# Optimization experiments

Hardware: AMD Instinct MI355X
Metric: run time of the kernel (lower is better)

Reference implementation:

```python
import jax, jax.numpy as jnp
import numpy as np

B, M, T, R, N_IN, O, K = 2, 20000, 8, 5, 64, 128, 4  # batch, verts, N_theta, N_rho, in, out, kernels


def setup_inputs() -> dict:
    key = jax.random.key(0)
    k1, k2, k3, k4 = jax.random.split(key, 4)
    signal = jax.random.normal(k1, (B, M, N_IN), dtype=jnp.float32)
    u = jax.random.uniform(k2, (B, M, T, R, 3), dtype=jnp.float32, minval=1e-3, maxval=1.0)
    bary_weights = u / jnp.sum(u, axis=-1, keepdims=True)  # barycentric: sum to 1
    bary_indices = jax.random.randint(k3, (B, M, T, R, 3), 0, M, dtype=jnp.int32)
    # glorot-ish scale for (amt_kernel, N_theta, N_rho, out, in) weight tensor
    kernel = jax.random.normal(k4, (K, T, R, O, N_IN), dtype=jnp.float32) * 0.05
    return {"signal": signal, "bary_weights": bary_weights,
            "bary_indices": bary_indices, "kernel": kernel}


def reference(signal, bary_weights, bary_indices, kernel):
    # signal: (B, m, n); bary_weights/indices: (B, m, T, R, 3); kernel: (K, T, R, o, n)
    Ksum = jnp.sum(kernel, axis=0)                      # sum over kernels k: (T, R, o, n)
    T_ = kernel.shape[1]
    j = jnp.arange(T_)
    rot = (j[None, :] + j[:, None]) % T_                # rot[r, j] = (j + r) % T
    Krot = Ksum[rot]                                    # (T_r, T_j, R, o, n)

    def one(sig, w, idx):
        g = sig[idx]                                    # gather: (m, T, R, 3, n)
        x = jnp.einsum('mtrc,mtrcn->mtrn', w, g)        # barycentric pullback (m, T, R, n)
        conv = jnp.einsum('rjion,mjin->rmo', Krot, x)   # per-rotation conv (T_r, m, o)
        a = jax.nn.relu(conv)
        norms = jnp.linalg.norm(a, axis=-1)             # (T_r, m)
        best = jnp.argmax(norms, axis=0)                # (m,)
        return jnp.take_along_axis(a, best[None, :, None], axis=0)[0]  # angular max pool (m, o)

    return jax.vmap(one)(signal, bary_weights, bary_indices)
```

## Files before the change

### kernel.cpp

```cpp
#include <hip/hip_runtime.h>
#include <hip/hip_bf16.h>


typedef _Float16 f16;
typedef _Float16 f16x8 __attribute__((ext_vector_type(8)));
typedef float f32x4 __attribute__((ext_vector_type(4)));

#define B_   2
#define M_   20000
#define T_   8
#define R_   5
#define NIN  64
#define O_   128
#define K_   4

#define PTS   (B_*M_)
#define PTSPAD 40192
#define KSEG  2560
#define KPHY  5120
#define KLOG  7680
#define NQ    1024
#define SCALE 16.0f
#define INVSS (1.0f/(SCALE*SCALE))

#define BM    256
#define BK    64
#define TS    (KLOG/BK)

__global__ void k_ksum(const float* __restrict__ kern, float* __restrict__ ksum) {
    int i = blockIdx.x * 256 + threadIdx.x;
    const int total = T_ * R_ * O_ * NIN;
    if (i >= total) return;
    float s = 0.f;
#pragma unroll
    for (int k = 0; k < K_; k++) s += kern[k * total + i];
    ksum[i] = s;
}

__global__ void k_wt(const float* __restrict__ ksum, f16* __restrict__ wt) {
    int idx = blockIdx.x * 256 + threadIdx.x;
    const int total = NQ * KSEG;
    if (idx >= total) return;
    int q = idx / KSEG;
    int k = idx - q * KSEG;
    int r = q >> 7, o = q & 127;
    int j = k / 320;
    int rem = k - j * 320;
    int i = rem >> 6, n = rem & 63;
    int t = (j + r) & 7;
    float v = SCALE * ksum[((((t * R_ + i) * O_ + o) << 6) + n)];
    f16 hi = (f16)v;
    f16 lo = (f16)(v - (float)hi);
    f16* row = wt + (size_t)q * KLOG;
    row[k] = hi;
    row[k + KSEG] = hi;
    row[k + 2 * KSEG] = lo;
}

__global__ void k_interp(const float* __restrict__ sig, const float* __restrict__ bw,
                         const int* __restrict__ bi, f16* __restrict__ X,
                         int pt0, int rows_pad) {
    int nwaves = gridDim.x * 4;
    int wav = (blockIdx.x * 256 + threadIdx.x) >> 6;
    int lane = threadIdx.x & 63;
    int ntask = rows_pad * T_;
    for (int task = wav; task < ntask; task += nwaves) {
        int tu = __builtin_amdgcn_readfirstlane(task);
        int lr = tu >> 3;
        int j = tu & 7;
        int pt = pt0 + lr;
        f16* rowp = X + (size_t)lr * KPHY + j * 320;
        if (pt >= PTS) {
#pragma unroll
            for (int i = 0; i < R_; i++) {
                rowp[i * 64 + lane] = (f16)0.f;
                rowp[KSEG + i * 64 + lane] = (f16)0.f;
            }
            continue;
        }
        int b = (pt >= M_) ? 1 : 0;
        const float* sb = sig + (size_t)b * M_ * NIN;
        const float* wp = bw + (size_t)pt * 120 + j * 15;
        const int* ip = bi + (size_t)pt * 120 + j * 15;
#pragma unroll
        for (int i = 0; i < R_; i++) {
            float w0 = wp[i * 3], w1 = wp[i * 3 + 1], w2 = wp[i * 3 + 2];
            int i0 = ip[i * 3], i1 = ip[i * 3 + 1], i2 = ip[i * 3 + 2];
            float x = w0 * sb[(size_t)i0 * NIN + lane];
            x = fmaf(w1, sb[(size_t)i1 * NIN + lane], x);
            x = fmaf(w2, sb[(size_t)i2 * NIN + lane], x);
            x *= SCALE;
            f16 hi = (f16)x;
            f16 lo = (f16)(x - (float)hi);
            rowp[i * 64 + lane] = hi;
            rowp[KSEG + i * 64 + lane] = lo;
        }
    }
}

__global__ __launch_bounds__(512, 1) void k_gemm(
    const f16* __restrict__ X, const f16* __restrict__ WT,
    float* __restrict__ conv, float* __restrict__ norms, int pt0) {
    __shared__ __align__(16) f16 As[2][256 * 64];
    __shared__ __align__(16) f16 Bs[2][256 * 64];
    __shared__ float sred[4][256];

    int nwg = gridDim.x;
    int bq = nwg >> 3, br_ = nwg & 7;
    int xcd = blockIdx.x & 7, slot = blockIdx.x >> 3;
    int logical = (xcd < br_ ? xcd * (bq + 1) : br_ * (bq + 1) + (xcd - br_) * bq) + slot;
    int mblk = logical >> 2, nb = logical & 3;
    const int m0 = mblk * BM;
    const int n0 = nb * 256;

    const int t = threadIdx.x;
    const int w = t >> 6, lane = t & 63;
    const int wr = w >> 2, wc = w & 3;
    const int lq = lane >> 4, lr16 = lane & 15;
    const int fr = lr16 & 7;
    const int src_off = (((t & 7) ^ ((t >> 3) & 7)) << 3);

    f32x4 acc[8][4];
#pragma unroll
    for (int a = 0; a < 8; a++)
#pragma unroll
        for (int b = 0; b < 4; b++) acc[a][b] = (f32x4){0.f, 0.f, 0.f, 0.f};

    const f16* pA = X + (size_t)(m0 + (t >> 3)) * KPHY + src_off;
    const f16* pB = WT + (size_t)(n0 + (t >> 3)) * KLOG + src_off;

#define STAGE(S, BUF) do {                                                            \
        int k0_ = (S) * BK;                                                           \
        int kA_ = k0_ - ((k0_ >= KPHY) ? KPHY : 0);           \
        _Pragma("unroll")                                                             \
        for (int i_ = 0; i_ < 4; i_++)                                                \
            __builtin_amdgcn_global_load_lds(                                         \
                (const __attribute__((address_space(1))) void*)(pA + kA_ + (size_t)i_ * 64 * KPHY), \
                (__attribute__((address_space(3))) void*)(&As[BUF][t * 8 + i_ * 4096]), 16, 0, 0); \
        _Pragma("unroll")                                                             \
        for (int i_ = 0; i_ < 4; i_++)                                                \
            __builtin_amdgcn_global_load_lds(                                         \
                (const __attribute__((address_space(1))) void*)(pB + k0_ + (size_t)i_ * 64 * KLOG), \
                (__attribute__((address_space(3))) void*)(&Bs[BUF][t * 8 + i_ * 4096]), 16, 0, 0); \
    } while (0)

    STAGE(0, 0);

    for (int s = 0; s < TS; ++s) {
        int cur = s & 1;
        if (s + 1 < TS) {
            STAGE(s + 1, cur ^ 1);
            asm volatile("s_waitcnt vmcnt(8)" ::: "memory");
        } else {
            asm volatile("s_waitcnt vmcnt(0)" ::: "memory");
        }
        __builtin_amdgcn_s_barrier();
        __builtin_amdgcn_sched_barrier(0);

        const f16* Ac = &As[cur][0];
        const f16* Bc = &Bs[cur][0];
#pragma unroll
        for (int kk = 0; kk < 2; ++kk) {
            const int cho = ((kk * 4 + lq) ^ fr) << 3;
            f16x8 af[8], bf[4];
#pragma unroll
            for (int mf = 0; mf < 8; mf++)
                af[mf] = *(const f16x8*)(Ac + (wr * 128 + mf * 16 + lr16) * 64 + cho);
#pragma unroll
            for (int nf = 0; nf < 4; nf++)
                bf[nf] = *(const f16x8*)(Bc + (wc * 64 + nf * 16 + lr16) * 64 + cho);
#pragma unroll
            for (int mf = 0; mf < 8; mf++)
#pragma unroll
                for (int nf = 0; nf < 4; nf++)
                    acc[mf][nf] = __builtin_amdgcn_mfma_f32_16x16x32_f16(af[mf], bf[nf], acc[mf][nf], 0, 0, 0);
        }
        __builtin_amdgcn_sched_barrier(0);
        __builtin_amdgcn_s_barrier();
    }
#undef STAGE

#pragma unroll
    for (int mf = 0; mf < 8; mf++)
#pragma unroll
        for (int nf = 0; nf < 4; nf++)
#pragma unroll
            for (int jj = 0; jj < 4; jj++)
                acc[mf][nf][jj] = fmaxf(acc[mf][nf][jj], 0.f);

#pragma unroll
    for (int mf = 0; mf < 8; mf++)
#pragma unroll
        for (int jj = 0; jj < 4; jj++) {
            int rowl = wr * 128 + mf * 16 + lq * 4 + jj;
            float s = 0.f;
#pragma unroll
            for (int nf = 0; nf < 4; nf++) {
                float v = acc[mf][nf][jj];
                s = fmaf(v, v, s);
                conv[(size_t)(m0 + rowl) * NQ + n0 + wc * 64 + nf * 16 + lr16] = v;
            }
            s += __shfl_xor(s, 1, 64);
            s += __shfl_xor(s, 2, 64);
            s += __shfl_xor(s, 4, 64);
            s += __shfl_xor(s, 8, 64);
            if (lr16 == 0) sred[wc][rowl] = s;
        }
    __syncthreads();
    if (t < 256) {
        float e = sred[0][t] + sred[1][t];
        float o = sred[2][t] + sred[3][t];
        float2* np = (float2*)&norms[(size_t)(pt0 + m0 + t) * 8 + nb * 2];
        *np = make_float2(e, o);
    }
}

__global__ void k_select(const float* __restrict__ conv, const float* __restrict__ norms,
                         float* __restrict__ out, int pt0, int rows) {
    int nwaves = gridDim.x * 4;
    int wav = (blockIdx.x * 256 + threadIdx.x) >> 6;
    int lane = threadIdx.x & 63;
    for (int task = wav; task < rows; task += nwaves) {
        int tu = __builtin_amdgcn_readfirstlane(task);
        int pt = pt0 + tu;
        if (pt >= PTS) continue;
        const float* np = norms + (size_t)pt * 8;
        float bs = np[0];
        int br = 0;
#pragma unroll
        for (int r = 1; r < 8; r++) {
            float v = np[r];
            if (v > bs) { bs = v; br = r; }
        }
        const float2 v = *(const float2*)&conv[(size_t)tu * NQ + br * 128 + lane * 2];
        float2 o;
        o.x = v.x * INVSS;
        o.y = v.y * INVSS;
        *(float2*)&out[(size_t)pt * O_ + lane * 2] = o;
    }
}

extern "C" void kernel_launch(void* const* d_in, const int* in_sizes, int n_in,
                              void* d_out, int out_size, void* d_ws, size_t ws_size,
                              hipStream_t stream) {
    const float* sig = (const float*)d_in[0];
    const float* bw = (const float*)d_in[1];
    const int* bi = (const int*)d_in[2];
    const float* kern = (const float*)d_in[3];
    float* out = (float*)d_out;
    char* ws = (char*)d_ws;

    const size_t sz_ksum = (size_t)T_ * R_ * O_ * NIN * sizeof(float);
    const size_t sz_wt = (size_t)NQ * KLOG * sizeof(f16);
    const size_t sz_norms = (size_t)PTSPAD * 8 * sizeof(float);
    float* ksum = (float*)ws;
    f16* WT = (f16*)(ws + sz_ksum);
    float* norms = (float*)(ws + sz_ksum + sz_wt);
    char* dyn = ws + sz_ksum + sz_wt + sz_norms;

    size_t persist = sz_ksum + sz_wt + sz_norms;
    size_t avail = (ws_size > persist) ? (ws_size - persist) : 0;
    long maxrows = (long)(avail / (size_t)(KPHY * 2 + NQ * 4));
    int chunk = (int)((maxrows / BM) * BM);
    if (chunk < BM) chunk = BM;
    if (chunk > PTSPAD) chunk = PTSPAD;

    f16* X = (f16*)dyn;
    float* conv = (float*)(dyn + (size_t)chunk * KPHY * sizeof(f16));

    k_ksum<<<(T_ * R_ * O_ * NIN + 255) / 256, 256, 0, stream>>>(kern, ksum);
    k_wt<<<(NQ * KSEG + 255) / 256, 256, 0, stream>>>(ksum, WT);

    for (int pt0 = 0; pt0 < PTS; pt0 += chunk) {
        int rem = PTS - pt0;
        int rows = (rem < chunk) ? rem : chunk;
        int rows_pad = (rows + BM - 1) & ~(BM - 1);
        k_interp<<<4096, 256, 0, stream>>>(sig, bw, bi, X, pt0, rows_pad);
        k_gemm<<<(rows_pad / BM) * 4, 512, 0, stream>>>(X, WT, conv, norms, pt0);
        k_select<<<2048, 256, 0, stream>>>(conv, norms, out, pt0, rows);
    }
}
```

Baseline: 1.457 ms.

## Restructure GEMM main loop into finely interleaved load/MFMA phases with priorities

```diff
diff --git a/kernel.cpp b/kernel.cpp
--- a/kernel.cpp
+++ b/kernel.cpp
@@ -98,6 +98,10 @@
     }
 }
 
+#define SBAR()  __builtin_amdgcn_s_barrier()
+#define SCHED() __builtin_amdgcn_sched_barrier(0)
+#define LGKM0() asm volatile("s_waitcnt lgkmcnt(0)" ::: "memory")
+
 __global__ __launch_bounds__(512, 1) void k_gemm(
     const f16* __restrict__ X, const f16* __restrict__ WT,
     float* __restrict__ conv, float* __restrict__ norms, int pt0) {
@@ -129,56 +133,108 @@
     const f16* pA = X + (size_t)(m0 + (t >> 3)) * KPHY + src_off;
     const f16* pB = WT + (size_t)(n0 + (t >> 3)) * KLOG + src_off;
 
-#define STAGE(S, BUF) do {                                                            \
-        int k0_ = (S) * BK;                                                           \
+#define GLA(Q, BUF, KT) do {                                                          \
+        int k0_ = (KT) * BK;                                                          \
         int kA_ = k0_ - ((k0_ >= KPHY) ? KPHY : 0);           \
-        _Pragma("unroll")                                                             \
-        for (int i_ = 0; i_ < 4; i_++)                                                \
-            __builtin_amdgcn_global_load_lds(                                         \
-                (const __attribute__((address_space(1))) void*)(pA + kA_ + (size_t)i_ * 64 * KPHY), \
-                (__attribute__((address_space(3))) void*)(&As[BUF][t * 8 + i_ * 4096]), 16, 0, 0); \
-        _Pragma("unroll")                                                             \
-        for (int i_ = 0; i_ < 4; i_++)                                                \
-            __builtin_amdgcn_global_load_lds(                                         \
-                (const __attribute__((address_space(1))) void*)(pB + k0_ + (size_t)i_ * 64 * KLOG), \
-                (__attribute__((address_space(3))) void*)(&Bs[BUF][t * 8 + i_ * 4096]), 16, 0, 0); \
+        __builtin_amdgcn_global_load_lds(                                             \
+            (const __attribute__((address_space(1))) void*)(pA + kA_ + (size_t)(Q) * 64 * KPHY), \
+            (__attribute__((address_space(3))) void*)(&As[BUF][(Q) * 4096 + t * 8]), 16, 0, 0); \
     } while (0)
-
-    STAGE(0, 0);
-
-    for (int s = 0; s < TS; ++s) {
-        int cur = s & 1;
-        if (s + 1 < TS) {
-            STAGE(s + 1, cur ^ 1);
-            asm volatile("s_waitcnt vmcnt(8)" ::: "memory");
-        } else {
-            asm volatile("s_waitcnt vmcnt(0)" ::: "memory");
-        }
-        __builtin_amdgcn_s_barrier();
-        __builtin_amdgcn_sched_barrier(0);
-
-        const f16* Ac = &As[cur][0];
-        const f16* Bc = &Bs[cur][0];
-#pragma unroll
-        for (int kk = 0; kk < 2; ++kk) {
-            const int cho = ((kk * 4 + lq) ^ fr) << 3;
-            f16x8 af[8], bf[4];
-#pragma unroll
-            for (int mf = 0; mf < 8; mf++)
-                af[mf] = *(const f16x8*)(Ac + (wr * 128 + mf * 16 + lr16) * 64 + cho);
+#define GLB(Q, BUF, KT) do {                                                          \
+        int k0_ = (KT) * BK;                                                          \
+        __builtin_amdgcn_global_load_lds(                                             \
+            (const __attribute__((address_space(1))) void*)(pB + k0_ + (size_t)(Q) * 64 * KLOG), \
+            (__attribute__((address_space(3))) void*)(&Bs[BUF][(Q) * 4096 + t * 8]), 16, 0, 0); \
+    } while (0)
+
+    GLA(0, 0, 0); GLA(1, 0, 0); GLA(2, 0, 0); GLA(3, 0, 0);
+    GLB(0, 0, 0); GLB(1, 0, 0); GLB(2, 0, 0); GLB(3, 0, 0);
+    GLA(0, 1, 1); GLA(2, 1, 1);
+    GLB(0, 1, 1); GLB(1, 1, 1); GLB(2, 1, 1); GLB(3, 1, 1);
+    asm volatile("s_waitcnt vmcnt(6)" ::: "memory");
+    SBAR(); SCHED();
+
+    f16x8 af[4], bf[4], bg[4];
+    for (int kt = 0; kt < TS; ++kt) {
+        const int b = kt & 1;
+        const f16* Ac = &As[b][0];
+        const f16* Bc = &Bs[b][0];
+        const int cho0 = (lq ^ fr) << 3;
+        const int cho1 = ((4 + lq) ^ fr) << 3;
+
+#pragma unroll
+        for (int mf = 0; mf < 4; mf++)
+            af[mf] = *(const f16x8*)(Ac + (wr * 128 + mf * 16 + lr16) * 64 + cho0);
+#pragma unroll
+        for (int nf = 0; nf < 4; nf++)
+            bf[nf] = *(const f16x8*)(Bc + (wc * 64 + nf * 16 + lr16) * 64 + cho0);
+        if (kt + 1 < TS) { GLA(1, b ^ 1, kt + 1); GLA(3, b ^ 1, kt + 1); }
+        SBAR(); SCHED();
+        LGKM0(); SCHED();
+        __builtin_amdgcn_s_setprio(1);
+#pragma unroll
+        for (int mf = 0; mf < 4; mf++)
 #pragma unroll
             for (int nf = 0; nf < 4; nf++)
-                bf[nf] = *(const f16x8*)(Bc + (wc * 64 + nf * 16 + lr16) * 64 + cho);
-#pragma unroll
-            for (int mf = 0; mf < 8; mf++)
-#pragma unroll
-                for (int nf = 0; nf < 4; nf++)
-                    acc[mf][nf] = __builtin_amdgcn_mfma_f32_16x16x32_f16(af[mf], bf[nf], acc[mf][nf], 0, 0, 0);
-        }
-        __builtin_amdgcn_sched_barrier(0);
-        __builtin_amdgcn_s_barrier();
-    }
-#undef STAGE
+                acc[mf][nf] = __builtin_amdgcn_mfma_f32_16x16x32_f16(af[mf], bf[nf], acc[mf][nf], 0, 0, 0);
+        __builtin_amdgcn_s_setprio(0); SCHED();
+        if (kt < TS - 1) asm volatile("s_waitcnt vmcnt(8)" ::: "memory");
+        else             asm volatile("s_waitcnt vmcnt(0)" ::: "memory");
+        SBAR(); SCHED();
+
+#pragma unroll
+        for (int mf = 0; mf < 4; mf++)
+            af[mf] = *(const f16x8*)(Ac + (wr * 128 + 64 + mf * 16 + lr16) * 64 + cho0);
+        SBAR(); SCHED();
+        LGKM0(); SCHED();
+        __builtin_amdgcn_s_setprio(1);
+#pragma unroll
+        for (int mf = 0; mf < 4; mf++)
+#pragma unroll
+            for (int nf = 0; nf < 4; nf++)
+                acc[4 + mf][nf] = __builtin_amdgcn_mfma_f32_16x16x32_f16(af[mf], bf[nf], acc[4 + mf][nf], 0, 0, 0);
+        __builtin_amdgcn_s_setprio(0); SCHED();
+        SBAR(); SCHED();
+
+#pragma unroll
+        for (int mf = 0; mf < 4; mf++)
+            af[mf] = *(const f16x8*)(Ac + (wr * 128 + mf * 16 + lr16) * 64 + cho1);
+#pragma unroll
+        for (int nf = 0; nf < 4; nf++)
+            bg[nf] = *(const f16x8*)(Bc + (wc * 64 + nf * 16 + lr16) * 64 + cho1);
+        SBAR(); SCHED();
+        LGKM0(); SCHED();
+        __builtin_amdgcn_s_setprio(1);
+#pragma unroll
+        for (int mf = 0; mf < 4; mf++)
+#pragma unroll
+            for (int nf = 0; nf < 4; nf++)
+                acc[mf][nf] = __builtin_amdgcn_mfma_f32_16x16x32_f16(af[mf], bg[nf], acc[mf][nf], 0, 0, 0);
+        __builtin_amdgcn_s_setprio(0); SCHED();
+        SBAR(); SCHED();
+
+#pragma unroll
+        for (int mf = 0; mf < 4; mf++)
+            af[mf] = *(const f16x8*)(Ac + (wr * 128 + 64 + mf * 16 + lr16) * 64 + cho1);
+        if (kt + 2 < TS) {
+            GLA(0, b, kt + 2); GLA(2, b, kt + 2);
+            GLB(0, b, kt + 2); GLB(1, b, kt + 2); GLB(2, b, kt + 2); GLB(3, b, kt + 2);
+        }
+        SBAR(); SCHED();
+        LGKM0(); SCHED();
+        __builtin_amdgcn_s_setprio(1);
+#pragma unroll
+        for (int mf = 0; mf < 4; mf++)
+#pragma unroll
+            for (int nf = 0; nf < 4; nf++)
+                acc[4 + mf][nf] = __builtin_amdgcn_mfma_f32_16x16x32_f16(af[mf], bg[nf], acc[4 + mf][nf], 0, 0, 0);
+        __builtin_amdgcn_s_setprio(0); SCHED();
+        if (kt < TS - 2)       asm volatile("s_waitcnt vmcnt(8)" ::: "memory");
+        else if (kt == TS - 2) asm volatile("s_waitcnt vmcnt(2)" ::: "memory");
+        SBAR(); SCHED();
+    }
+#undef GLA
+#undef GLB
 
 #pragma unroll
     for (int mf = 0; mf < 8; mf++)
@@ -275,7 +331,7 @@
         int rem = PTS - pt0;
         int rows = (rem < chunk) ? rem : chunk;
         int rows_pad = (rows + BM - 1) & ~(BM - 1);
-        k_interp<<<4096, 256, 0, stream>>>(sig, bw, bi, X, pt0, rows_pad);
+        k_interp<<<8192, 256, 0, stream>>>(sig, bw, bi, X, pt0, rows_pad);
         k_gemm<<<(rows_pad / BM) * 4, 512, 0, stream>>>(X, WT, conv, norms, pt0);
         k_select<<<2048, 256, 0, stream>>>(conv, norms, out, pt0, rows);
     }
```

After: 1.351 ms. -7.3%, faster.
